# Kernel optimization log

Hardware: AMD Instinct MI355X
Metric: run time of the kernel (lower is better)

## Reference

```python
import jax, jax.numpy as jnp
import numpy as np
import math

B, L, DM, H, DK, DV, T, PW = 2, 512, 256, 4, 64, 64, 8, 8


def setup_inputs() -> dict:
    key = jax.random.key(0)
    ks = jax.random.split(key, 16)
    q = jax.random.normal(ks[0], (B, L, DM), jnp.float32)
    k = jax.random.normal(ks[1], (B, L, DM), jnp.float32)
    v = jax.random.normal(ks[2], (B, L, DM), jnp.float32)
    # sorted timestamps in [0, 100]
    t_in = jnp.sort(jax.random.uniform(ks[3], (B, L), jnp.float32) * 100.0, axis=-1)
    c = jax.random.randint(ks[4], (B, L), 0, T).astype(jnp.int32)  # no padding tokens
    mask = jnp.broadcast_to(jnp.triu(jnp.ones((L, L), bool), 1)[None], (B, L, L))  # causal
    s_in = 1.0 / math.sqrt(DM)
    Wq = jax.random.normal(ks[5], (DM, H * DK), jnp.float32) * s_in
    Wk = jax.random.normal(ks[6], (DM, H * DK), jnp.float32) * s_in
    Wv = jax.random.normal(ks[7], (DM, H * DV), jnp.float32) * s_in
    Wo = jax.random.normal(ks[8], (H * DV, DM), jnp.float32) / math.sqrt(H * DV)
    ln_g = jnp.ones((DM,), jnp.float32)
    ln_b = jnp.zeros((DM,), jnp.float32)
    # per-(type, head) phi MLP: Linear(1->PW), GELU, Linear(PW->PW), GELU, Linear(PW->1)
    W0 = jax.random.normal(ks[9], (T, H, PW, 1), jnp.float32) * 0.1
    b0 = jax.random.normal(ks[10], (T, H, PW), jnp.float32) * 0.1
    W1 = jax.random.normal(ks[11], (T, H, PW, PW), jnp.float32) * 0.3
    b1 = jax.random.normal(ks[12], (T, H, PW), jnp.float32) * 0.1
    Wf = jax.random.normal(ks[13], (T, H, 1, PW), jnp.float32) * 0.3
    bf = jax.random.normal(ks[14], (T, H, 1), jnp.float32) * 0.1
    return dict(q=q, k=k, v=v, t_in=t_in, c=c, mask=mask, ln_g=ln_g, ln_b=ln_b,
                Wq=Wq, Wk=Wk, Wv=Wv, Wo=Wo, W0=W0, b0=b0, W1=W1, b1=b1, Wf=Wf, bf=bf)


def _gelu(x):
    return jax.nn.gelu(x, approximate=False)


def _forward(q, k, v, t_in, c, mask, ln_g, ln_b, Wq, Wk, Wv, Wo, W0, b0, W1, b1, Wf, bf):
    Bb, Ll, dm = q.shape
    num_types, Hh, pw, _ = W0.shape
    dk = Wq.shape[1] // Hh
    dv = Wv.shape[1] // Hh
    scale = math.sqrt(dk)
    residual = q
    # pre-LayerNorm on q only (normalize_before=True)
    mu = jnp.mean(q, -1, keepdims=True)
    var = jnp.mean((q - mu) ** 2, -1, keepdims=True)
    qn = (q - mu) / jnp.sqrt(var + 1e-6) * ln_g + ln_b
    qh = (qn @ Wq).reshape(Bb, Ll, Hh, dk).transpose(0, 2, 1, 3)  # (B,H,L,dk)
    kh = (k @ Wk).reshape(Bb, Ll, Hh, dk).transpose(0, 2, 1, 3)
    vh = (v @ Wv).reshape(Bb, Ll, Hh, dv).transpose(0, 2, 1, 3)
    delta = t_in[:, :, None] - t_in[:, None, :]  # (B,Li,Lj)
    valid = c < num_types
    vmask = valid[:, :, None] & valid[:, None, :]  # (B,Li,Lj)
    cs = jnp.clip(c, 0, num_types - 1)
    # gather per-token phi params -> leading dims (B,L,H,...)
    W0g = W0[cs][..., 0]          # (B,L,H,pw)
    b0g = b0[cs]                  # (B,L,H,pw)
    W1g = W1[cs]                  # (B,L,H,pw,pw)  [out,in]
    b1g = b1[cs]                  # (B,L,H,pw)
    Wfg = Wf[cs][:, :, :, 0, :]   # (B,L,H,pw)
    bfg = bf[cs][..., 0]          # (B,L,H)
    # phiQ[b,h,i,j] = phi_{c_i,h}(delta_ij)
    hq = _gelu(delta[:, :, None, :, None] * W0g[:, :, :, None, :] + b0g[:, :, :, None, :])  # (B,Li,H,Lj,pw)
    hq = _gelu(jnp.einsum('bihjw,bihuw->bihju', hq, W1g) + b1g[:, :, :, None, :])
    phiQ = jnp.einsum('bihjw,bihw->bihj', hq, Wfg) + bfg[:, :, :, None]  # (B,Li,H,Lj)
    phiQ = jnp.where(vmask[:, :, None, :], phiQ, 0.0).transpose(0, 2, 1, 3)  # (B,H,Li,Lj)
    # phiK[b,h,i,j] = phi_{c_j,h}(delta_ij)
    hk = _gelu(delta[:, :, :, None, None] * W0g[:, None, :, :, :] + b0g[:, None, :, :, :])  # (B,Li,Lj,H,pw)
    hk = _gelu(jnp.einsum('bijhw,bjhuw->bijhu', hk, W1g) + b1g[:, None, :, :, :])
    phiK = jnp.einsum('bijhw,bjhw->bijh', hk, Wfg) + bfg[:, None, :, :]  # (B,Li,Lj,H)
    phiK = jnp.where(vmask[:, :, :, None], phiK, 0.0).transpose(0, 3, 1, 2)  # (B,H,Li,Lj)
    # scores[b,h,i,j] = (q_i . k_j) * phiQ * phiK / scale  (equivalent to q_mod*k_mod sum)
    scores = jnp.einsum('bhid,bhjd->bhij', qh, kh) * phiQ * phiK / scale
    scores = jnp.where(mask[:, None, :, :], -jnp.inf, scores)
    attn = jax.nn.softmax(scores, axis=-1)
    # out_heads[b,h,i,d] = sum_j attn * phiK * v_j  (equivalent to einsum with v_mod)
    out_heads = jnp.einsum('bhij,bhjd->bhid', attn * phiK, vh)
    out = out_heads.transpose(0, 2, 1, 3).reshape(Bb, Ll, Hh * dv) @ Wo
    return out + residual


def reference(q, k, v, t_in, c, mask, ln_g, ln_b, Wq, Wk, Wv, Wo, W0, b0, W1, b1, Wf, bf):
    return _forward(q, k, v, t_in, c, mask, ln_g, ln_b, Wq, Wk, Wv, Wo, W0, b0, W1, b1, Wf, bf)
```

## Files before the change

### kernel.cpp

```cpp
#include <hip/hip_runtime.h>
#include <math.h>

#define B_  2
#define L_  512
#define DM_ 256
#define H_  4
#define DK_ 64
#define DV_ 64
#define T_  8
#define PW_ 8
#define NTAB 4096

typedef unsigned int uint;

__device__ __forceinline__ unsigned short f2b(float x) {
    uint u = __float_as_uint(x);
    u += 0x7fffu + ((u >> 16) & 1u);
    return (unsigned short)(u >> 16);
}
__device__ __forceinline__ float bl(uint u)  { return __uint_as_float(u << 16); }
__device__ __forceinline__ float bh_(uint u) { return __uint_as_float(u & 0xffff0000u); }

__device__ __forceinline__ float gelu_fast(float x) {
    const float z  = x * 0.70710678118654752440f;
    const float az = fabsf(z);
    const float t  = __builtin_amdgcn_rcpf(fmaf(0.3275911f, az, 1.0f));
    float p = fmaf(t, 1.061405429f, -1.453152027f);
    p = fmaf(t, p, 1.421413741f);
    p = fmaf(t, p, -0.284496736f);
    p = fmaf(t, p, 0.254829592f);
    p *= t;
    const float e  = __expf(-az * az);
    float er = fmaf(-p, e, 1.0f);
    er = copysignf(er, z);
    return 0.5f * x * (1.0f + er);
}

__device__ __forceinline__ float phi_eval_u(
        const float w0r[8], const float b0r[8], const float4* __restrict__ W14,
        const float b1r[8], const float wfr[8], float bfv, float delta) {
    float h1[PW_];
#pragma unroll
    for (int w = 0; w < PW_; ++w)
        h1[w] = gelu_fast(fmaf(delta, w0r[w], b0r[w]));
    float out = bfv;
#pragma unroll
    for (int u = 0; u < PW_; ++u) {
        const float4 c0 = W14[u * 2];
        const float4 c1 = W14[u * 2 + 1];
        float a = b1r[u];
        a = fmaf(c0.x, h1[0], a); a = fmaf(c0.y, h1[1], a);
        a = fmaf(c0.z, h1[2], a); a = fmaf(c0.w, h1[3], a);
        a = fmaf(c1.x, h1[4], a); a = fmaf(c1.y, h1[5], a);
        a = fmaf(c1.z, h1[6], a); a = fmaf(c1.w, h1[7], a);
        out = fmaf(wfr[u], gelu_fast(a), out);
    }
    return out;
}

__device__ __forceinline__ float tab_lerp(const float* __restrict__ tab, float delta) {
    float x = delta * ((float)(NTAB - 1) / 100.0f);
    x = fminf(fmaxf(x, 0.0f), (float)(NTAB - 1) - 0.001f);
    const int i0 = (int)x;
    const float f = x - (float)i0;
    const float a = tab[i0];
    const float b = tab[i0 + 1];
    return fmaf(b - a, f, a);
}

__global__ __launch_bounds__(256) void prep_kernel(
        const float* __restrict__ q, const float* __restrict__ k,
        const float* __restrict__ v, const float* __restrict__ ln_g,
        const float* __restrict__ ln_b, const float* __restrict__ Wq,
        const float* __restrict__ Wk, const float* __restrict__ Wv,
        const float* __restrict__ W0, const float* __restrict__ b0,
        const float* __restrict__ W1, const float* __restrict__ b1,
        const float* __restrict__ Wf, const float* __restrict__ bfp,
        float* __restrict__ qh, uint* __restrict__ khT,
        uint* __restrict__ vh8, float* __restrict__ tabs) {
    __shared__ __align__(16) float smem[8 * DM_];
    const int tid = threadIdx.x, lane = tid & 63, wv = tid >> 6;
    const int bx = blockIdx.x;

    if (bx < 512) {
        const int th = bx >> 4;
        const int p = (bx & 15) * 256 + tid;
        if (tid < 64) smem[tid] = W1[th * 64 + tid];
        float w0r[8], b0r[8], b1r[8], wfr[8];
#pragma unroll
        for (int w = 0; w < 8; ++w) {
            w0r[w] = W0[th * 8 + w]; b0r[w] = b0[th * 8 + w];
            b1r[w] = b1[th * 8 + w]; wfr[w] = Wf[th * 8 + w];
        }
        const float bfv = bfp[th];
        __syncthreads();
        const float delta = (float)p * (100.0f / (float)(NTAB - 1));
        tabs[th * NTAB + p] = phi_eval_u(w0r, b0r,
                                         reinterpret_cast<const float4*>(smem),
                                         b1r, wfr, bfv, delta);
    } else if (bx < 1024) {
        const bool isQ = (bx < 768);
        const int bid = isQ ? (bx - 512) : (bx - 768);
        float (*xr)[DM_] = reinterpret_cast<float (*)[DM_]>(smem);
        const int row0 = bid * 4;
        const int b = row0 >> 9;
        const int lrow0 = row0 & (L_ - 1);
        const float* src = isQ ? q : k;
        const float* W   = isQ ? Wq : Wk;
        for (int x = tid; x < 4 * DM_; x += 256)
            xr[x >> 8][x & 255] = src[(size_t)row0 * DM_ + x];
        __syncthreads();
        if (isQ) {
            const int r = wv;
            float x0 = xr[r][lane], x1 = xr[r][lane + 64];
            float x2 = xr[r][lane + 128], x3 = xr[r][lane + 192];
            float s = x0 + x1 + x2 + x3;
#pragma unroll
            for (int off = 32; off; off >>= 1) s += __shfl_xor(s, off);
            const float mean = s * (1.0f / 256.0f);
            x0 -= mean; x1 -= mean; x2 -= mean; x3 -= mean;
            float s2 = x0 * x0 + x1 * x1 + x2 * x2 + x3 * x3;
#pragma unroll
            for (int off = 32; off; off >>= 1) s2 += __shfl_xor(s2, off);
            const float rstd = rsqrtf(s2 * (1.0f / 256.0f) + 1e-6f);
            xr[r][lane]       = x0 * rstd * ln_g[lane]       + ln_b[lane];
            xr[r][lane + 64]  = x1 * rstd * ln_g[lane + 64]  + ln_b[lane + 64];
            xr[r][lane + 128] = x2 * rstd * ln_g[lane + 128] + ln_b[lane + 128];
            xr[r][lane + 192] = x3 * rstd * ln_g[lane + 192] + ln_b[lane + 192];
            __syncthreads();
        }
        float acc[4] = {0, 0, 0, 0};
#pragma unroll 8
        for (int kk = 0; kk < DM_; ++kk) {
            const float w = W[(size_t)kk * DM_ + tid];
#pragma unroll
            for (int r = 0; r < 4; ++r) acc[r] = fmaf(xr[r][kk], w, acc[r]);
        }
        if (isQ) {
#pragma unroll
            for (int r = 0; r < 4; ++r)
                qh[(size_t)(row0 + r) * DM_ + tid] = acc[r];
        } else {
            __syncthreads();
            unsigned short* sbuf = reinterpret_cast<unsigned short*>(smem);
#pragma unroll
            for (int r = 0; r < 4; ++r)
                sbuf[tid * 4 + r] = f2b(acc[r]);
            __syncthreads();
            if (tid < 128) {
                const int jl = tid & 3;
                const int g = tid >> 2;
                const int h2 = g >> 3, d8 = g & 7;
                unsigned short e[8];
#pragma unroll
                for (int ee = 0; ee < 8; ++ee)
                    e[ee] = sbuf[(h2 * 64 + d8 * 8 + ee) * 4 + jl];
                uint4 o;
                o.x = (uint)e[0] | ((uint)e[1] << 16);
                o.y = (uint)e[2] | ((uint)e[3] << 16);
                o.z = (uint)e[4] | ((uint)e[5] << 16);
                o.w = (uint)e[6] | ((uint)e[7] << 16);
                reinterpret_cast<uint4*>(khT)[
                    ((size_t)(b * H_ + h2) * 8 + d8) * L_ + lrow0 + jl] = o;
            }
        }
    } else {
        const int bid = bx - 1024;
        float (*xr)[DM_] = reinterpret_cast<float (*)[DM_]>(smem);
        const int row0 = bid * 8;
        const int b = row0 >> 9;
        const int lrow0 = row0 & (L_ - 1);
        for (int x = tid; x < 8 * DM_; x += 256)
            xr[x >> 8][x & 255] = v[(size_t)row0 * DM_ + x];
        __syncthreads();
        float acc[8] = {0, 0, 0, 0, 0, 0, 0, 0};
#pragma unroll 4
        for (int kk = 0; kk < DM_; ++kk) {
            const float w = Wv[(size_t)kk * DM_ + tid];
#pragma unroll
            for (int r = 0; r < 8; ++r) acc[r] = fmaf(xr[r][kk], w, acc[r]);
        }
        const int h = tid >> 6, d = tid & 63;
        const int bh = b * H_ + h;
        uint4 w4;
        w4.x = (uint)f2b(acc[0]) | ((uint)f2b(acc[1]) << 16);
        w4.y = (uint)f2b(acc[2]) | ((uint)f2b(acc[3]) << 16);
        w4.z = (uint)f2b(acc[4]) | ((uint)f2b(acc[5]) << 16);
        w4.w = (uint)f2b(acc[6]) | ((uint)f2b(acc[7]) << 16);
        reinterpret_cast<uint4*>(vh8)[((size_t)bh * 64 + (lrow0 >> 3)) * 64 + d] = w4;
    }
}

__global__ __launch_bounds__(64) void attn_kernel(
        const float* __restrict__ qh, const uint* __restrict__ khT,
        const uint* __restrict__ vh8, const float* __restrict__ t_in,
        const int* __restrict__ c, const float* __restrict__ tabs,
        float* __restrict__ oh) {
    __shared__ __align__(16) float qs[64];
    __shared__ __align__(16) float sw[L_];

    const int lane = threadIdx.x;
    const int unit = blockIdx.x;
    const int bh = unit & 7;
    const int b = bh >> 2, h = bh & 3;
    const int i = (L_ - 1) - (unit >> 3);
    const int row = b * L_ + i;

    qs[lane] = qh[(size_t)row * DM_ + h * DK_ + lane];
    const float ti = t_in[row];
    const int ciw = c[row];
    const bool vi = (ciw < T_);
    const float* tabQ = tabs + (size_t)(min(max(ciw, 0), T_ - 1) * H_ + h) * NTAB;
    __syncthreads();

    const float4* qs4 = reinterpret_cast<const float4*>(qs);
    const uint4* kT8 = reinterpret_cast<const uint4*>(khT) + (size_t)bh * 8 * L_;
    const float* tbase = t_in + b * L_;
    const int* cbase = c + b * L_;
    const int tmax = i >> 6;

    float s[8], pk[8];
    float m = -INFINITY;
#pragma unroll
    for (int t = 0; t < 8; ++t) {
        s[t] = -INFINITY; pk[t] = 0.0f;
        if (t <= tmax) {
            const int j = t * 64 + lane;
            const bool act = (j <= i);
            const float tj = tbase[j];
            const int cjw = cbase[j];
            const float* tabK = tabs + (size_t)(min(max(cjw, 0), T_ - 1) * H_ + h) * NTAB;
            const float delta = ti - tj;
            const float pq = vi ? tab_lerp(tabQ, delta) : 0.0f;
            const float pkv = (cjw < T_) ? tab_lerp(tabK, delta) : 0.0f;
            float dot = 0.0f;
#pragma unroll
            for (int d8 = 0; d8 < 8; ++d8) {
                const uint4 ku = kT8[(size_t)d8 * L_ + j];
                const float4 qa = qs4[2 * d8];
                const float4 qb = qs4[2 * d8 + 1];
                dot = fmaf(qa.x, bl(ku.x), fmaf(qa.y, bh_(ku.x),
                      fmaf(qa.z, bl(ku.y), fmaf(qa.w, bh_(ku.y), dot))));
                dot = fmaf(qb.x, bl(ku.z), fmaf(qb.y, bh_(ku.z),
                      fmaf(qb.z, bl(ku.w), fmaf(qb.w, bh_(ku.w), dot))));
            }
            if (act) { s[t] = dot * pq * pkv * 0.125f; pk[t] = pkv; }
            m = fmaxf(m, s[t]);
        }
    }
#pragma unroll
    for (int off = 32; off; off >>= 1) m = fmaxf(m, __shfl_xor(m, off));

    float l = 0.0f;
#pragma unroll
    for (int t = 0; t < 8; ++t) {
        if (t <= tmax) {
            const float e = __expf(s[t] - m);
            l += e;
            sw[t * 64 + lane] = e * pk[t];
        }
    }
#pragma unroll
    for (int off = 32; off; off >>= 1) l += __shfl_xor(l, off);
    __syncthreads();

    const uint4* vb = reinterpret_cast<const uint4*>(vh8) + (size_t)bh * 64 * 64 + lane;
    const int j8max = i >> 3;
    float a0 = 0.0f, a1 = 0.0f;
    for (int j8 = 0; j8 <= j8max; ++j8) {
        const uint4 u = vb[(size_t)j8 * 64];
        const float4 w0 = *reinterpret_cast<const float4*>(&sw[j8 * 8]);
        const float4 w1 = *reinterpret_cast<const float4*>(&sw[j8 * 8 + 4]);
        a0 = fmaf(w0.x, bl(u.x), fmaf(w0.y, bh_(u.x),
             fmaf(w0.z, bl(u.y), fmaf(w0.w, bh_(u.y), a0))));
        a1 = fmaf(w1.x, bl(u.z), fmaf(w1.y, bh_(u.z),
             fmaf(w1.z, bl(u.w), fmaf(w1.w, bh_(u.w), a1))));
    }
    const float acc = a0 + a1;
    oh[(size_t)row * DM_ + h * DV_ + lane] = vi ? acc / l : 0.0f;
}

__global__ __launch_bounds__(256) void out4_kernel(const float* __restrict__ oh,
                                                   const float* __restrict__ Wo,
                                                   const float* __restrict__ q,
                                                   float* __restrict__ out) {
    __shared__ __align__(16) float xr[4][DM_];
    const int tid = threadIdx.x;
    const int row0 = blockIdx.x * 4;
    for (int x = tid; x < 4 * DM_; x += 256)
        xr[x >> 8][x & 255] = oh[(size_t)row0 * DM_ + x];
    __syncthreads();
    float acc[4] = {0, 0, 0, 0};
#pragma unroll 8
    for (int kk = 0; kk < DM_; ++kk) {
        const float w = Wo[(size_t)kk * DM_ + tid];
#pragma unroll
        for (int r = 0; r < 4; ++r) acc[r] = fmaf(xr[r][kk], w, acc[r]);
    }
#pragma unroll
    for (int r = 0; r < 4; ++r)
        out[(size_t)(row0 + r) * DM_ + tid] = acc[r] + q[(size_t)(row0 + r) * DM_ + tid];
}

extern "C" void kernel_launch(void* const* d_in, const int* in_sizes, int n_in,
                              void* d_out, int out_size, void* d_ws, size_t ws_size,
                              hipStream_t stream) {
    const float* q    = (const float*)d_in[0];
    const float* k    = (const float*)d_in[1];
    const float* v    = (const float*)d_in[2];
    const float* t_in = (const float*)d_in[3];
    const int*   c    = (const int*)d_in[4];
    const float* ln_g = (const float*)d_in[6];
    const float* ln_b = (const float*)d_in[7];
    const float* Wq   = (const float*)d_in[8];
    const float* Wk   = (const float*)d_in[9];
    const float* Wv   = (const float*)d_in[10];
    const float* Wo   = (const float*)d_in[11];
    const float* W0   = (const float*)d_in[12];
    const float* b0   = (const float*)d_in[13];
    const float* W1   = (const float*)d_in[14];
    const float* b1   = (const float*)d_in[15];
    const float* Wf   = (const float*)d_in[16];
    const float* bf   = (const float*)d_in[17];
    float* outp = (float*)d_out;

    const size_t SZ = (size_t)B_ * L_ * DM_;
    float* ws = (float*)d_ws;
    float* qh   = ws;
    uint*  khT  = (uint*)(ws + SZ);
    uint*  vh8  = (uint*)(ws + SZ + 131072);
    float* oh   = ws + SZ + 262144;
    float* tabs = ws + 2 * SZ + 262144;

    prep_kernel<<<dim3(1152), dim3(256), 0, stream>>>(
        q, k, v, ln_g, ln_b, Wq, Wk, Wv,
        W0, b0, W1, b1, Wf, bf, qh, khT, vh8, tabs);
    attn_kernel<<<dim3(4096), dim3(64), 0, stream>>>(
        qh, khT, vh8, t_in, c, tabs, oh);
    out4_kernel<<<dim3(256), dim3(256), 0, stream>>>(oh, Wo, q, outp);
}
```

Baseline: 47.01 us.

## Fuse output projection into attention kernel via per-row-group completion counters

Removes the separate output-projection kernel. Each attention block increments an atomic counter for its group of 4 rows. The last of the 16 contributing blocks (4 rows × 4 heads) reads the group's head outputs back and computes the Wo projection plus the residual with float4 loads. The counters are zeroed in the prep kernel. This saves a kernel launch and lets the projection overlap with attention work that is still running, at the cost of thread fences, atomics, extra shared memory per attention block and a serial tail in the finishing block.

```diff
diff --git a/kernel.cpp b/kernel.cpp
--- a/kernel.cpp
+++ b/kernel.cpp
@@ -77,12 +77,14 @@
         const float* __restrict__ W1, const float* __restrict__ b1,
         const float* __restrict__ Wf, const float* __restrict__ bfp,
         float* __restrict__ qh, uint* __restrict__ khT,
-        uint* __restrict__ vh8, float* __restrict__ tabs) {
+        uint* __restrict__ vh8, float* __restrict__ tabs,
+        uint* __restrict__ cnt) {
     __shared__ __align__(16) float smem[8 * DM_];
     const int tid = threadIdx.x, lane = tid & 63, wv = tid >> 6;
     const int bx = blockIdx.x;
 
     if (bx < 512) {
+        if (bx == 0) cnt[tid] = 0;
         const int th = bx >> 4;
         const int p = (bx & 15) * 256 + tid;
         if (tid < 64) smem[tid] = W1[th * 64 + tid];
@@ -195,9 +197,12 @@
         const float* __restrict__ qh, const uint* __restrict__ khT,
         const uint* __restrict__ vh8, const float* __restrict__ t_in,
         const int* __restrict__ c, const float* __restrict__ tabs,
-        float* __restrict__ oh) {
+        float* __restrict__ oh, const float* __restrict__ Wo,
+        const float* __restrict__ qres, float* __restrict__ outp,
+        uint* __restrict__ cnt) {
     __shared__ __align__(16) float qs[64];
     __shared__ __align__(16) float sw[L_];
+    __shared__ __align__(16) float xr2[4 * DM_];
 
     const int lane = threadIdx.x;
     const int unit = blockIdx.x;
@@ -278,28 +283,42 @@
     }
     const float acc = a0 + a1;
     oh[(size_t)row * DM_ + h * DV_ + lane] = vi ? acc / l : 0.0f;
-}
-
-__global__ __launch_bounds__(256) void out4_kernel(const float* __restrict__ oh,
-                                                   const float* __restrict__ Wo,
-                                                   const float* __restrict__ q,
-                                                   float* __restrict__ out) {
-    __shared__ __align__(16) float xr[4][DM_];
-    const int tid = threadIdx.x;
-    const int row0 = blockIdx.x * 4;
-    for (int x = tid; x < 4 * DM_; x += 256)
-        xr[x >> 8][x & 255] = oh[(size_t)row0 * DM_ + x];
-    __syncthreads();
-    float acc[4] = {0, 0, 0, 0};
-#pragma unroll 8
-    for (int kk = 0; kk < DM_; ++kk) {
-        const float w = Wo[(size_t)kk * DM_ + tid];
-#pragma unroll
-        for (int r = 0; r < 4; ++r) acc[r] = fmaf(xr[r][kk], w, acc[r]);
-    }
-#pragma unroll
-    for (int r = 0; r < 4; ++r)
-        out[(size_t)(row0 + r) * DM_ + tid] = acc[r] + q[(size_t)(row0 + r) * DM_ + tid];
+
+    __threadfence();
+    uint old = 0;
+    if (lane == 0) old = atomicAdd(&cnt[row >> 2], 1u);
+    old = __shfl(old, 0);
+    if (old == 15u) {
+        __threadfence();
+        const int row0 = row & ~3;
+        for (int x = lane; x < 4 * DM_; x += 64)
+            xr2[x] = oh[(size_t)row0 * DM_ + x];
+        __syncthreads();
+        float a4[4][4] = {{0,0,0,0},{0,0,0,0},{0,0,0,0},{0,0,0,0}};
+        for (int kk = 0; kk < DM_; ++kk) {
+            const float4 w = *reinterpret_cast<const float4*>(
+                &Wo[(size_t)kk * DM_ + lane * 4]);
+#pragma unroll
+            for (int r = 0; r < 4; ++r) {
+                const float xv = xr2[r * DM_ + kk];
+                a4[r][0] = fmaf(xv, w.x, a4[r][0]);
+                a4[r][1] = fmaf(xv, w.y, a4[r][1]);
+                a4[r][2] = fmaf(xv, w.z, a4[r][2]);
+                a4[r][3] = fmaf(xv, w.w, a4[r][3]);
+            }
+        }
+#pragma unroll
+        for (int r = 0; r < 4; ++r) {
+            const float4 res = *reinterpret_cast<const float4*>(
+                &qres[(size_t)(row0 + r) * DM_ + lane * 4]);
+            float4 o;
+            o.x = a4[r][0] + res.x;
+            o.y = a4[r][1] + res.y;
+            o.z = a4[r][2] + res.z;
+            o.w = a4[r][3] + res.w;
+            *reinterpret_cast<float4*>(&outp[(size_t)(row0 + r) * DM_ + lane * 4]) = o;
+        }
+    }
 }
 
 extern "C" void kernel_launch(void* const* d_in, const int* in_sizes, int n_in,
@@ -331,11 +350,11 @@
     uint*  vh8  = (uint*)(ws + SZ + 131072);
     float* oh   = ws + SZ + 262144;
     float* tabs = ws + 2 * SZ + 262144;
+    uint*  cnt  = (uint*)(ws + 2 * SZ + 262144 + 131072);
 
     prep_kernel<<<dim3(1152), dim3(256), 0, stream>>>(
         q, k, v, ln_g, ln_b, Wq, Wk, Wv,
-        W0, b0, W1, b1, Wf, bf, qh, khT, vh8, tabs);
+        W0, b0, W1, b1, Wf, bf, qh, khT, vh8, tabs, cnt);
     attn_kernel<<<dim3(4096), dim3(64), 0, stream>>>(
-        qh, khT, vh8, t_in, c, tabs, oh);
-    out4_kernel<<<dim3(256), dim3(256), 0, stream>>>(oh, Wo, q, outp);
-}
+        qh, khT, vh8, t_in, c, tabs, oh, Wo, q, outp, cnt);
+}
```

Result: slower. 155.2 us (+230.2%).
